# Performance work log

Hardware: AMD Instinct MI355X
Metric: run time of the kernel (lower is better)

Reference implementation:

```python
import jax, jax.numpy as jnp
import numpy as np

NEG_INF = -9.0e15  # matches torch's -9000000000000000.0 mask value
ALPHA = 0.2        # LeakyReLU negative slope


def setup_inputs() -> dict:
    key = jax.random.key(0)
    k1, k2, k3, k4 = jax.random.split(key, 4)
    N, F_in, F_out = 8192, 128, 128
    x = jax.random.normal(k1, (N, F_in), dtype=jnp.float32)
    adj = jax.random.randint(k2, (N, N), 0, 2, dtype=jnp.int32)
    W = jax.random.normal(k3, (F_in, F_out), dtype=jnp.float32) * (1.0 / np.sqrt(F_in))
    a = jax.random.normal(k4, (2 * F_out, 1), dtype=jnp.float32) * (1.0 / np.sqrt(2 * F_out))
    return {"x": x, "adj": adj, "W": W, "a": a}


def reference(x, adj, W, a):
    # h = W(input): [N, F_out]
    h = x @ W
    F_out = h.shape[1]
    # a([h_i || h_j]) = h_i . a[:F] + h_j . a[F:]  -- identical math to the
    # original NxNx2F concat, without materializing it.
    a_src = a[:F_out, 0]   # coefficients on the row (i) node
    a_dst = a[F_out:, 0]   # coefficients on the column (j) node
    s_src = h @ a_src      # [N]
    s_dst = h @ a_dst      # [N]
    e = jax.nn.leaky_relu(s_src[:, None] + s_dst[None, :], negative_slope=ALPHA)  # [N, N]
    e = jnp.where(adj > 0, e, jnp.float32(NEG_INF))
    attention = jax.nn.softmax(e, axis=1)
    # dropout omitted (identity at eval) for a deterministic baseline
    h_prime = attention @ h  # [N, F_out]
    return h_prime
```

## Files before the change

### kernel.cpp

```cpp
#include <hip/hip_runtime.h>

#define N 8192
#define F 128
#define ALPHA 0.2f
#define NSPLIT 4

typedef __attribute__((ext_vector_type(8))) short short8;
typedef __attribute__((ext_vector_type(4))) float f32x4;
typedef unsigned short u16;

__device__ __forceinline__ u16 f2bf(float f) {
    unsigned int u = __float_as_uint(f);
    u += 0x7fff + ((u >> 16) & 1);
    return (u16)(u >> 16);
}

__global__ __launch_bounds__(256) void gemm_h(const float* __restrict__ x,
                                              const float* __restrict__ W,
                                              const float* __restrict__ aa,
                                              u16* __restrict__ hT,
                                              float* __restrict__ ssrc,
                                              float* __restrict__ sdst) {
    __shared__ float xs[32 * 128];
    __shared__ float Wsh[32 * 128];
    const int t = threadIdx.x;
    const int i0 = blockIdx.x * 32;
    const int c4 = (t & 31) * 4;
    const int r8 = t >> 5;

#pragma unroll
    for (int p = 0; p < 4; ++p) {
        int rr = p * 8 + r8;
        *(float4*)&xs[rr * 128 + c4] = *(const float4*)&x[(size_t)(i0 + rr) * 128 + c4];
    }

    const int tx = t & 31, ty = t >> 5;
    const int r0 = ty * 4, c0 = tx * 4;
    float acc[4][4] = {};

    for (int kc = 0; kc < 4; ++kc) {
        __syncthreads();
#pragma unroll
        for (int p = 0; p < 4; ++p) {
            int k = p * 8 + r8;
            *(float4*)&Wsh[k * 128 + c4] = *(const float4*)&W[(kc * 32 + k) * 128 + c4];
        }
        __syncthreads();
#pragma unroll 4
        for (int k = 0; k < 32; k += 4) {
            float xr[4][4];
#pragma unroll
            for (int rr = 0; rr < 4; ++rr)
                *(float4*)xr[rr] = *(const float4*)&xs[(r0 + rr) * 128 + kc * 32 + k];
#pragma unroll
            for (int kk = 0; kk < 4; ++kk) {
                float4 wv = *(const float4*)&Wsh[(k + kk) * 128 + c0];
#pragma unroll
                for (int rr = 0; rr < 4; ++rr) {
                    acc[rr][0] += xr[rr][kk] * wv.x;
                    acc[rr][1] += xr[rr][kk] * wv.y;
                    acc[rr][2] += xr[rr][kk] * wv.z;
                    acc[rr][3] += xr[rr][kk] * wv.w;
                }
            }
        }
    }

#pragma unroll
    for (int rr = 0; rr < 4; ++rr)
#pragma unroll
        for (int cc = 0; cc < 4; ++cc)
            hT[(size_t)(c0 + cc) * N + (i0 + r0 + rr)] = f2bf(acc[rr][cc]);

    float4 asv = *(const float4*)&aa[c0];
    float4 adv = *(const float4*)&aa[F + c0];
#pragma unroll
    for (int rr = 0; rr < 4; ++rr) {
        float vs = acc[rr][0] * asv.x + acc[rr][1] * asv.y + acc[rr][2] * asv.z + acc[rr][3] * asv.w;
        float vd = acc[rr][0] * adv.x + acc[rr][1] * adv.y + acc[rr][2] * adv.z + acc[rr][3] * adv.w;
#pragma unroll
        for (int off = 16; off >= 1; off >>= 1) {
            vs += __shfl_down(vs, off, 32);
            vd += __shfl_down(vd, off, 32);
        }
        if (tx == 0) {
            ssrc[i0 + r0 + rr] = vs;
            sdst[i0 + r0 + rr] = vd;
        }
    }
}

__global__ __launch_bounds__(256, 3) void attn_mfma(const int* __restrict__ adj,
                                                    const u16* __restrict__ hT,
                                                    const float* __restrict__ ssrc,
                                                    const float* __restrict__ sdst,
                                                    float* __restrict__ out,
                                                    float* __restrict__ pacc,
                                                    float* __restrict__ pS) {
    __shared__ short8 wsh[2][4][64];
    __shared__ float srow[2][2][16];

    const int t = threadIdx.x;
    const int w = t >> 6, L = t & 63;
    const int quad = L >> 4, l16 = L & 15;
    const int i0 = blockIdx.x * 32;
    const int split = blockIdx.y;
    const int JW = N / NSPLIT;
    const int jbase = split * JW;
    const int NC = JW / 64;

    const int rt = w & 1, ks = w >> 1;
    const int fragid = rt * 2 + ks;
    const int prow = i0 + rt * 16 + l16;
    const float s_i = ssrc[prow];

    const int* pA = adj + (size_t)prow * N + jbase + ks * 32 + quad * 8;
    const float* pD = sdst + jbase + ks * 32 + quad * 8;
    const u16* pB = hT + (size_t)(w * 32 + l16) * N + jbase + quad * 8;

    f32x4 acc[2][2];
#pragma unroll
    for (int a = 0; a < 2; ++a)
#pragma unroll
        for (int b = 0; b < 2; ++b) acc[a][b] = 0.f;
    float rsum = 0.f;

    auto compute_write = [&](int buf, int4 a0, int4 a1, float4 d0, float4 d1) {
        const int m[8] = {a0.x, a0.y, a0.z, a0.w, a1.x, a1.y, a1.z, a1.w};
        const float d[8] = {d0.x, d0.y, d0.z, d0.w, d1.x, d1.y, d1.z, d1.w};
        float wv[8];
#pragma unroll
        for (int k = 0; k < 8; ++k) {
            float z = s_i + d[k];
            float e = __expf(fmaxf(z, ALPHA * z));
            wv[k] = (m[k] > 0) ? e : 0.f;
        }
        union { unsigned int u[4]; short8 s8; } pk;
        float s = 0.f;
#pragma unroll
        for (int p = 0; p < 4; ++p) {
            unsigned int r;
            asm("v_cvt_pk_bf16_f32 %0, %1, %2" : "=v"(r) : "v"(wv[2 * p]), "v"(wv[2 * p + 1]));
            pk.u[p] = r;
            s += __uint_as_float(r << 16);
            s += __uint_as_float(r & 0xffff0000u);
        }
        rsum += s;
        wsh[buf][fragid][L] = pk.s8;
    };

    int4 aN0 = *(const int4*)(pA);
    int4 aN1 = *(const int4*)(pA + 4);
    int4 aP0 = *(const int4*)(pA + 64);
    int4 aP1 = *(const int4*)(pA + 68);
    float4 dN0 = *(const float4*)(pD);
    float4 dN1 = *(const float4*)(pD + 4);
    compute_write(0, aN0, aN1, dN0, dN1);
    aN0 = aP0; aN1 = aP1;
    aP0 = *(const int4*)(pA + 128);
    aP1 = *(const int4*)(pA + 132);
    dN0 = *(const float4*)(pD + 64);
    dN1 = *(const float4*)(pD + 68);

    short8 Bbuf[2][2];
#pragma unroll
    for (int c2 = 0; c2 < 2; ++c2)
#pragma unroll
        for (int kb = 0; kb < 2; ++kb)
            Bbuf[c2][kb] = *(const short8*)(pB + (size_t)c2 * 16 * N + kb * 32);

    for (int c = 1; c < NC; ++c) {
        __syncthreads();
        const int coff = c * 64;

        short8 Bload[2][2];
#pragma unroll
        for (int c2 = 0; c2 < 2; ++c2)
#pragma unroll
            for (int kb = 0; kb < 2; ++kb)
                Bload[c2][kb] = *(const short8*)(pB + (size_t)c2 * 16 * N + kb * 32 + coff);

        compute_write(c & 1, aN0, aN1, dN0, dN1);

        aN0 = aP0; aN1 = aP1;
        const int ca = (c + 2 < NC) ? c + 2 : NC - 1;
        aP0 = *(const int4*)(pA + ca * 64);
        aP1 = *(const int4*)(pA + ca * 64 + 4);
        const int cd = (c + 1 < NC) ? c + 1 : NC - 1;
        dN0 = *(const float4*)(pD + cd * 64);
        dN1 = *(const float4*)(pD + cd * 64 + 4);

        short8 af[4];
#pragma unroll
        for (int fs = 0; fs < 4; ++fs) af[fs] = wsh[(c - 1) & 1][fs][L];
#pragma unroll
        for (int c2 = 0; c2 < 2; ++c2)
#pragma unroll
            for (int rc = 0; rc < 2; ++rc)
#pragma unroll
                for (int kb = 0; kb < 2; ++kb)
                    acc[c2][rc] = __builtin_amdgcn_mfma_f32_16x16x32_bf16(
                        af[rc * 2 + kb], Bbuf[c2][kb], acc[c2][rc], 0, 0, 0);

#pragma unroll
        for (int c2 = 0; c2 < 2; ++c2)
#pragma unroll
            for (int kb = 0; kb < 2; ++kb) Bbuf[c2][kb] = Bload[c2][kb];
    }

    __syncthreads();
    {
        short8 af[4];
#pragma unroll
        for (int fs = 0; fs < 4; ++fs) af[fs] = wsh[(NC - 1) & 1][fs][L];
#pragma unroll
        for (int c2 = 0; c2 < 2; ++c2)
#pragma unroll
            for (int rc = 0; rc < 2; ++rc)
#pragma unroll
                for (int kb = 0; kb < 2; ++kb)
                    acc[c2][rc] = __builtin_amdgcn_mfma_f32_16x16x32_bf16(
                        af[rc * 2 + kb], Bbuf[c2][kb], acc[c2][rc], 0, 0, 0);
    }

    float* dst = split ? pacc + (size_t)(split - 1) * N * F : out;
#pragma unroll
    for (int c2 = 0; c2 < 2; ++c2) {
        const int col = (w * 2 + c2) * 16 + l16;
#pragma unroll
        for (int rc = 0; rc < 2; ++rc) {
            const int row0 = i0 + rc * 16 + quad * 4;
#pragma unroll
            for (int r = 0; r < 4; ++r)
                dst[(size_t)(row0 + r) * F + col] = acc[c2][rc][r];
        }
    }

    rsum += __shfl_xor(rsum, 16);
    rsum += __shfl_xor(rsum, 32);
    if (L < 16) srow[rt][ks][l16] = rsum;
    __syncthreads();
    if (t < 32) pS[split * N + i0 + t] = srow[t >> 4][0][t & 15] + srow[t >> 4][1][t & 15];
}

__global__ __launch_bounds__(256) void finalize(float* __restrict__ out,
                                                const float* __restrict__ pacc,
                                                const float* __restrict__ pS) {
    const int idx = (blockIdx.x * 256 + threadIdx.x) * 4;
    const int i = idx >> 7;
    const float inv = 1.0f / (pS[i] + pS[N + i] + pS[2 * N + i] + pS[3 * N + i]);
    float4 a0 = *(const float4*)&out[idx];
    float4 a1 = *(const float4*)&pacc[idx];
    float4 a2 = *(const float4*)&pacc[(size_t)N * F + idx];
    float4 a3 = *(const float4*)&pacc[2 * (size_t)N * F + idx];
    float4 o = {(a0.x + a1.x + a2.x + a3.x) * inv,
                (a0.y + a1.y + a2.y + a3.y) * inv,
                (a0.z + a1.z + a2.z + a3.z) * inv,
                (a0.w + a1.w + a2.w + a3.w) * inv};
    *(float4*)&out[idx] = o;
}

extern "C" void kernel_launch(void* const* d_in, const int* in_sizes, int n_in,
                              void* d_out, int out_size, void* d_ws, size_t ws_size,
                              hipStream_t stream) {
    (void)in_sizes; (void)n_in; (void)out_size; (void)ws_size;
    const float* x   = (const float*)d_in[0];
    const int*   adj = (const int*)d_in[1];
    const float* W   = (const float*)d_in[2];
    const float* a   = (const float*)d_in[3];
    float* out = (float*)d_out;

    u16* hT     = (u16*)d_ws;
    float* ssrc = (float*)(hT + (size_t)N * F);
    float* sdst = ssrc + N;
    float* pS   = sdst + N;
    float* pacc = pS + NSPLIT * N;

    gemm_h<<<N / 32, 256, 0, stream>>>(x, W, a, hT, ssrc, sdst);
    attn_mfma<<<dim3(N / 32, NSPLIT), 256, 0, stream>>>(adj, hT, ssrc, sdst, out, pacc, pS);
    finalize<<<(N * F / 4) / 256, 256, 0, stream>>>(out, pacc, pS);
}
```

Baseline: 417.5 us.

## Fuse split-K attention and finalize into one kernel with per-wave K slices

The attention kernel now gives each block 16 rows. Each of its four waves handles a quarter of the columns and keeps all 128 output features in registers, so the shared-memory weight exchange and the per-chunk barriers go away. The partial sums are reduced across waves through shared memory, normalized, and written directly. This removes the global partial-accumulator buffers and the separate finalize kernel. In exchange each wave loads all of hT per chunk with no reuse across waves, uses more registers (occupancy hint dropped to 2), and the grid has more blocks with half the rows each, so B-operand traffic from hT doubles.

```diff
diff --git a/kernel.cpp b/kernel.cpp
--- a/kernel.cpp
+++ b/kernel.cpp
@@ -3,7 +3,6 @@
 #define N 8192
 #define F 128
 #define ALPHA 0.2f
-#define NSPLIT 4
 
 typedef __attribute__((ext_vector_type(8))) short short8;
 typedef __attribute__((ext_vector_type(4))) float f32x4;
@@ -90,42 +89,34 @@
     }
 }
 
-__global__ __launch_bounds__(256, 3) void attn_mfma(const int* __restrict__ adj,
-                                                    const u16* __restrict__ hT,
-                                                    const float* __restrict__ ssrc,
-                                                    const float* __restrict__ sdst,
-                                                    float* __restrict__ out,
-                                                    float* __restrict__ pacc,
-                                                    float* __restrict__ pS) {
-    __shared__ short8 wsh[2][4][64];
-    __shared__ float srow[2][2][16];
+__global__ __launch_bounds__(256, 2) void attn_fused(const int* __restrict__ adj,
+                                                     const u16* __restrict__ hT,
+                                                     const float* __restrict__ ssrc,
+                                                     const float* __restrict__ sdst,
+                                                     float* __restrict__ out) {
+    __shared__ float accsh[4][16][132];
+    __shared__ float srow[4][16];
 
     const int t = threadIdx.x;
     const int w = t >> 6, L = t & 63;
     const int quad = L >> 4, l16 = L & 15;
-    const int i0 = blockIdx.x * 32;
-    const int split = blockIdx.y;
-    const int JW = N / NSPLIT;
-    const int jbase = split * JW;
-    const int NC = JW / 64;
-
-    const int rt = w & 1, ks = w >> 1;
-    const int fragid = rt * 2 + ks;
-    const int prow = i0 + rt * 16 + l16;
+    const int tile0 = blockIdx.x * 16;
+    const int prow = tile0 + l16;
+    const int JW = N / 4;
+    const int jbase = w * JW;
+    const int NC = JW / 32;
+
     const float s_i = ssrc[prow];
-
-    const int* pA = adj + (size_t)prow * N + jbase + ks * 32 + quad * 8;
-    const float* pD = sdst + jbase + ks * 32 + quad * 8;
-    const u16* pB = hT + (size_t)(w * 32 + l16) * N + jbase + quad * 8;
-
-    f32x4 acc[2][2];
-#pragma unroll
-    for (int a = 0; a < 2; ++a)
-#pragma unroll
-        for (int b = 0; b < 2; ++b) acc[a][b] = 0.f;
+    const int* pA = adj + (size_t)prow * N + jbase + quad * 8;
+    const float* pD = sdst + jbase + quad * 8;
+    const u16* pB = hT + (size_t)l16 * N + jbase + quad * 8;
+
+    f32x4 acc[8];
+#pragma unroll
+    for (int cg = 0; cg < 8; ++cg) acc[cg] = 0.f;
     float rsum = 0.f;
 
-    auto compute_write = [&](int buf, int4 a0, int4 a1, float4 d0, float4 d1) {
+    auto mk_frag = [&](int4 a0, int4 a1, float4 d0, float4 d1) -> short8 {
         const int m[8] = {a0.x, a0.y, a0.z, a0.w, a1.x, a1.y, a1.z, a1.w};
         const float d[8] = {d0.x, d0.y, d0.z, d0.w, d1.x, d1.y, d1.z, d1.w};
         float wv[8];
@@ -146,118 +137,73 @@
             s += __uint_as_float(r & 0xffff0000u);
         }
         rsum += s;
-        wsh[buf][fragid][L] = pk.s8;
+        return pk.s8;
     };
 
-    int4 aN0 = *(const int4*)(pA);
-    int4 aN1 = *(const int4*)(pA + 4);
-    int4 aP0 = *(const int4*)(pA + 64);
-    int4 aP1 = *(const int4*)(pA + 68);
-    float4 dN0 = *(const float4*)(pD);
-    float4 dN1 = *(const float4*)(pD + 4);
-    compute_write(0, aN0, aN1, dN0, dN1);
-    aN0 = aP0; aN1 = aP1;
-    aP0 = *(const int4*)(pA + 128);
-    aP1 = *(const int4*)(pA + 132);
-    dN0 = *(const float4*)(pD + 64);
-    dN1 = *(const float4*)(pD + 68);
-
-    short8 Bbuf[2][2];
-#pragma unroll
-    for (int c2 = 0; c2 < 2; ++c2)
-#pragma unroll
-        for (int kb = 0; kb < 2; ++kb)
-            Bbuf[c2][kb] = *(const short8*)(pB + (size_t)c2 * 16 * N + kb * 32);
-
-    for (int c = 1; c < NC; ++c) {
-        __syncthreads();
-        const int coff = c * 64;
-
-        short8 Bload[2][2];
-#pragma unroll
-        for (int c2 = 0; c2 < 2; ++c2)
-#pragma unroll
-            for (int kb = 0; kb < 2; ++kb)
-                Bload[c2][kb] = *(const short8*)(pB + (size_t)c2 * 16 * N + kb * 32 + coff);
-
-        compute_write(c & 1, aN0, aN1, dN0, dN1);
-
-        aN0 = aP0; aN1 = aP1;
-        const int ca = (c + 2 < NC) ? c + 2 : NC - 1;
-        aP0 = *(const int4*)(pA + ca * 64);
-        aP1 = *(const int4*)(pA + ca * 64 + 4);
+    int4 aA0 = *(const int4*)(pA);
+    int4 aA1 = *(const int4*)(pA + 4);
+    int4 aB0 = *(const int4*)(pA + 32);
+    int4 aB1 = *(const int4*)(pA + 36);
+    int4 aC0 = *(const int4*)(pA + 64);
+    int4 aC1 = *(const int4*)(pA + 68);
+    float4 dA0 = *(const float4*)(pD);
+    float4 dA1 = *(const float4*)(pD + 4);
+
+    for (int c = 0; c < NC; ++c) {
+        const int coff = c * 32;
+
+        const int ca = (c + 3 < NC) ? c + 3 : NC - 1;
         const int cd = (c + 1 < NC) ? c + 1 : NC - 1;
-        dN0 = *(const float4*)(pD + cd * 64);
-        dN1 = *(const float4*)(pD + cd * 64 + 4);
-
-        short8 af[4];
-#pragma unroll
-        for (int fs = 0; fs < 4; ++fs) af[fs] = wsh[(c - 1) & 1][fs][L];
-#pragma unroll
-        for (int c2 = 0; c2 < 2; ++c2)
-#pragma unroll
-            for (int rc = 0; rc < 2; ++rc)
-#pragma unroll
-                for (int kb = 0; kb < 2; ++kb)
-                    acc[c2][rc] = __builtin_amdgcn_mfma_f32_16x16x32_bf16(
-                        af[rc * 2 + kb], Bbuf[c2][kb], acc[c2][rc], 0, 0, 0);
-
-#pragma unroll
-        for (int c2 = 0; c2 < 2; ++c2)
-#pragma unroll
-            for (int kb = 0; kb < 2; ++kb) Bbuf[c2][kb] = Bload[c2][kb];
-    }
-
-    __syncthreads();
-    {
-        short8 af[4];
-#pragma unroll
-        for (int fs = 0; fs < 4; ++fs) af[fs] = wsh[(NC - 1) & 1][fs][L];
-#pragma unroll
-        for (int c2 = 0; c2 < 2; ++c2)
-#pragma unroll
-            for (int rc = 0; rc < 2; ++rc)
-#pragma unroll
-                for (int kb = 0; kb < 2; ++kb)
-                    acc[c2][rc] = __builtin_amdgcn_mfma_f32_16x16x32_bf16(
-                        af[rc * 2 + kb], Bbuf[c2][kb], acc[c2][rc], 0, 0, 0);
-    }
-
-    float* dst = split ? pacc + (size_t)(split - 1) * N * F : out;
-#pragma unroll
-    for (int c2 = 0; c2 < 2; ++c2) {
-        const int col = (w * 2 + c2) * 16 + l16;
-#pragma unroll
-        for (int rc = 0; rc < 2; ++rc) {
-            const int row0 = i0 + rc * 16 + quad * 4;
-#pragma unroll
-            for (int r = 0; r < 4; ++r)
-                dst[(size_t)(row0 + r) * F + col] = acc[c2][rc][r];
-        }
+        int4 nA0 = *(const int4*)(pA + ca * 32);
+        int4 nA1 = *(const int4*)(pA + ca * 32 + 4);
+        float4 nD0 = *(const float4*)(pD + cd * 32);
+        float4 nD1 = *(const float4*)(pD + cd * 32 + 4);
+
+        short8 Bv[8];
+#pragma unroll
+        for (int cg = 0; cg < 8; ++cg)
+            Bv[cg] = *(const short8*)(pB + (size_t)cg * 16 * N + coff);
+
+        short8 af = mk_frag(aA0, aA1, dA0, dA1);
+
+#pragma unroll
+        for (int cg = 0; cg < 8; ++cg)
+            acc[cg] = __builtin_amdgcn_mfma_f32_16x16x32_bf16(af, Bv[cg], acc[cg], 0, 0, 0);
+
+        aA0 = aB0; aA1 = aB1;
+        aB0 = aC0; aB1 = aC1;
+        aC0 = nA0; aC1 = nA1;
+        dA0 = nD0; dA1 = nD1;
     }
 
     rsum += __shfl_xor(rsum, 16);
     rsum += __shfl_xor(rsum, 32);
-    if (L < 16) srow[rt][ks][l16] = rsum;
+    if (L < 16) srow[w][l16] = rsum;
+
+#pragma unroll
+    for (int cg = 0; cg < 8; ++cg)
+#pragma unroll
+        for (int r = 0; r < 4; ++r)
+            accsh[w][quad * 4 + r][cg * 16 + l16] = acc[cg][r];
+
     __syncthreads();
-    if (t < 32) pS[split * N + i0 + t] = srow[t >> 4][0][t & 15] + srow[t >> 4][1][t & 15];
-}
-
-__global__ __launch_bounds__(256) void finalize(float* __restrict__ out,
-                                                const float* __restrict__ pacc,
-                                                const float* __restrict__ pS) {
-    const int idx = (blockIdx.x * 256 + threadIdx.x) * 4;
-    const int i = idx >> 7;
-    const float inv = 1.0f / (pS[i] + pS[N + i] + pS[2 * N + i] + pS[3 * N + i]);
-    float4 a0 = *(const float4*)&out[idx];
-    float4 a1 = *(const float4*)&pacc[idx];
-    float4 a2 = *(const float4*)&pacc[(size_t)N * F + idx];
-    float4 a3 = *(const float4*)&pacc[2 * (size_t)N * F + idx];
-    float4 o = {(a0.x + a1.x + a2.x + a3.x) * inv,
-                (a0.y + a1.y + a2.y + a3.y) * inv,
-                (a0.z + a1.z + a2.z + a3.z) * inv,
-                (a0.w + a1.w + a2.w + a3.w) * inv};
-    *(float4*)&out[idx] = o;
+
+#pragma unroll
+    for (int p = 0; p < 2; ++p) {
+        const int fid = t * 2 + p;
+        const int row = fid >> 5;
+        const int c4 = (fid & 31) * 4;
+        float4 s0 = *(const float4*)&accsh[0][row][c4];
+        float4 s1 = *(const float4*)&accsh[1][row][c4];
+        float4 s2 = *(const float4*)&accsh[2][row][c4];
+        float4 s3 = *(const float4*)&accsh[3][row][c4];
+        const float inv = 1.0f / (srow[0][row] + srow[1][row] + srow[2][row] + srow[3][row]);
+        float4 o = {(s0.x + s1.x + s2.x + s3.x) * inv,
+                    (s0.y + s1.y + s2.y + s3.y) * inv,
+                    (s0.z + s1.z + s2.z + s3.z) * inv,
+                    (s0.w + s1.w + s2.w + s3.w) * inv};
+        *(float4*)&out[(size_t)(tile0 + row) * F + c4] = o;
+    }
 }
 
 extern "C" void kernel_launch(void* const* d_in, const int* in_sizes, int n_in,
@@ -273,10 +219,7 @@
     u16* hT     = (u16*)d_ws;
     float* ssrc = (float*)(hT + (size_t)N * F);
     float* sdst = ssrc + N;
-    float* pS   = sdst + N;
-    float* pacc = pS + NSPLIT * N;
 
     gemm_h<<<N / 32, 256, 0, stream>>>(x, W, a, hT, ssrc, sdst);
-    attn_mfma<<<dim3(N / 32, NSPLIT), 256, 0, stream>>>(adj, hT, ssrc, sdst, out, pacc, pS);
-    finalize<<<(N * F / 4) / 256, 256, 0, stream>>>(out, pacc, pS);
-}
+    attn_fused<<<N / 16, 256, 0, stream>>>(adj, hT, ssrc, sdst, out);
+}
```

Result: slower. 485.0 us (+16.2%).

## Double attention row tile to 64 rows per block, reuse B fragments

Applied to the files above, without the earlier changes.

Each block now handles 64 rows instead of 32, with each wave computing weights for two row tiles and all waves doing MFMAs across four row tiles. This halves the number of loads of hT fragments per output row and reduces the block count. The adj prefetch depth drops from two chunks to one, and the MFMA step is issued before the weight computation for the next chunk. The occupancy hint drops from 3 to 2 because register use rises, and the grid is smaller.

```diff
diff --git a/kernel.cpp b/kernel.cpp
--- a/kernel.cpp
+++ b/kernel.cpp
@@ -90,42 +90,45 @@
     }
 }
 
-__global__ __launch_bounds__(256, 3) void attn_mfma(const int* __restrict__ adj,
+__global__ __launch_bounds__(256, 2) void attn_mfma(const int* __restrict__ adj,
                                                     const u16* __restrict__ hT,
                                                     const float* __restrict__ ssrc,
                                                     const float* __restrict__ sdst,
                                                     float* __restrict__ out,
                                                     float* __restrict__ pacc,
                                                     float* __restrict__ pS) {
-    __shared__ short8 wsh[2][4][64];
-    __shared__ float srow[2][2][16];
+    __shared__ short8 wsh[2][8][64];
+    __shared__ float srow[4][2][16];
 
     const int t = threadIdx.x;
     const int w = t >> 6, L = t & 63;
     const int quad = L >> 4, l16 = L & 15;
-    const int i0 = blockIdx.x * 32;
+    const int i0 = blockIdx.x * 64;
     const int split = blockIdx.y;
     const int JW = N / NSPLIT;
     const int jbase = split * JW;
     const int NC = JW / 64;
 
-    const int rt = w & 1, ks = w >> 1;
-    const int fragid = rt * 2 + ks;
-    const int prow = i0 + rt * 16 + l16;
-    const float s_i = ssrc[prow];
-
-    const int* pA = adj + (size_t)prow * N + jbase + ks * 32 + quad * 8;
+    const int ks = w & 1, rp = w >> 1;
+    const int prow0 = i0 + (rp * 2 + 0) * 16 + l16;
+    const int prow1 = i0 + (rp * 2 + 1) * 16 + l16;
+    const float s0 = ssrc[prow0];
+    const float s1 = ssrc[prow1];
+
+    const int* pA0 = adj + (size_t)prow0 * N + jbase + ks * 32 + quad * 8;
+    const int* pA1 = adj + (size_t)prow1 * N + jbase + ks * 32 + quad * 8;
     const float* pD = sdst + jbase + ks * 32 + quad * 8;
     const u16* pB = hT + (size_t)(w * 32 + l16) * N + jbase + quad * 8;
 
-    f32x4 acc[2][2];
+    f32x4 acc[2][4];
 #pragma unroll
     for (int a = 0; a < 2; ++a)
 #pragma unroll
-        for (int b = 0; b < 2; ++b) acc[a][b] = 0.f;
-    float rsum = 0.f;
-
-    auto compute_write = [&](int buf, int4 a0, int4 a1, float4 d0, float4 d1) {
+        for (int b = 0; b < 4; ++b) acc[a][b] = 0.f;
+    float rs0 = 0.f, rs1 = 0.f;
+
+    auto cw = [&](int buf, int fragid, float s_i, float& rsum,
+                  int4 a0, int4 a1, float4 d0, float4 d1) {
         const int m[8] = {a0.x, a0.y, a0.z, a0.w, a1.x, a1.y, a1.z, a1.w};
         const float d[8] = {d0.x, d0.y, d0.z, d0.w, d1.x, d1.y, d1.z, d1.w};
         float wv[8];
@@ -149,25 +152,25 @@
         wsh[buf][fragid][L] = pk.s8;
     };
 
-    int4 aN0 = *(const int4*)(pA);
-    int4 aN1 = *(const int4*)(pA + 4);
-    int4 aP0 = *(const int4*)(pA + 64);
-    int4 aP1 = *(const int4*)(pA + 68);
-    float4 dN0 = *(const float4*)(pD);
-    float4 dN1 = *(const float4*)(pD + 4);
-    compute_write(0, aN0, aN1, dN0, dN1);
-    aN0 = aP0; aN1 = aP1;
-    aP0 = *(const int4*)(pA + 128);
-    aP1 = *(const int4*)(pA + 132);
-    dN0 = *(const float4*)(pD + 64);
-    dN1 = *(const float4*)(pD + 68);
+    const int f0 = (rp * 2 + 0) * 2 + ks;
+    const int f1 = (rp * 2 + 1) * 2 + ks;
+
+    int4 aN00 = *(const int4*)(pA0);     int4 aN01 = *(const int4*)(pA0 + 4);
+    int4 aN10 = *(const int4*)(pA1);     int4 aN11 = *(const int4*)(pA1 + 4);
+    float4 dN0 = *(const float4*)(pD);   float4 dN1 = *(const float4*)(pD + 4);
+    cw(0, f0, s0, rs0, aN00, aN01, dN0, dN1);
+    cw(0, f1, s1, rs1, aN10, aN11, dN0, dN1);
 
     short8 Bbuf[2][2];
 #pragma unroll
     for (int c2 = 0; c2 < 2; ++c2)
 #pragma unroll
         for (int kb = 0; kb < 2; ++kb)
-            Bbuf[c2][kb] = *(const short8*)(pB + (size_t)c2 * 16 * N + kb * 32);
+            Bbuf[c2][kb] = *(const short8*)(pB + (size_t)(c2 * 16) * N + kb * 32);
+
+    aN00 = *(const int4*)(pA0 + 64);  aN01 = *(const int4*)(pA0 + 68);
+    aN10 = *(const int4*)(pA1 + 64);  aN11 = *(const int4*)(pA1 + 68);
+    dN0 = *(const float4*)(pD + 64);  dN1 = *(const float4*)(pD + 68);
 
     for (int c = 1; c < NC; ++c) {
         __syncthreads();
@@ -178,30 +181,31 @@
         for (int c2 = 0; c2 < 2; ++c2)
 #pragma unroll
             for (int kb = 0; kb < 2; ++kb)
-                Bload[c2][kb] = *(const short8*)(pB + (size_t)c2 * 16 * N + kb * 32 + coff);
-
-        compute_write(c & 1, aN0, aN1, dN0, dN1);
-
-        aN0 = aP0; aN1 = aP1;
-        const int ca = (c + 2 < NC) ? c + 2 : NC - 1;
-        aP0 = *(const int4*)(pA + ca * 64);
-        aP1 = *(const int4*)(pA + ca * 64 + 4);
-        const int cd = (c + 1 < NC) ? c + 1 : NC - 1;
-        dN0 = *(const float4*)(pD + cd * 64);
-        dN1 = *(const float4*)(pD + cd * 64 + 4);
-
-        short8 af[4];
-#pragma unroll
-        for (int fs = 0; fs < 4; ++fs) af[fs] = wsh[(c - 1) & 1][fs][L];
-#pragma unroll
-        for (int c2 = 0; c2 < 2; ++c2)
-#pragma unroll
-            for (int rc = 0; rc < 2; ++rc)
+                Bload[c2][kb] = *(const short8*)(pB + (size_t)(c2 * 16) * N + kb * 32 + coff);
+
+        const int cn = (c + 1 < NC) ? c + 1 : NC - 1;
+        int4 aP00 = *(const int4*)(pA0 + cn * 64);  int4 aP01 = *(const int4*)(pA0 + cn * 64 + 4);
+        int4 aP10 = *(const int4*)(pA1 + cn * 64);  int4 aP11 = *(const int4*)(pA1 + cn * 64 + 4);
+        float4 dP0 = *(const float4*)(pD + cn * 64);
+        float4 dP1 = *(const float4*)(pD + cn * 64 + 4);
+
+        short8 af[8];
+#pragma unroll
+        for (int fs = 0; fs < 8; ++fs) af[fs] = wsh[(c - 1) & 1][fs][L];
+#pragma unroll
+        for (int c2 = 0; c2 < 2; ++c2)
+#pragma unroll
+            for (int rt = 0; rt < 4; ++rt)
 #pragma unroll
                 for (int kb = 0; kb < 2; ++kb)
-                    acc[c2][rc] = __builtin_amdgcn_mfma_f32_16x16x32_bf16(
-                        af[rc * 2 + kb], Bbuf[c2][kb], acc[c2][rc], 0, 0, 0);
-
+                    acc[c2][rt] = __builtin_amdgcn_mfma_f32_16x16x32_bf16(
+                        af[rt * 2 + kb], Bbuf[c2][kb], acc[c2][rt], 0, 0, 0);
+
+        cw(c & 1, f0, s0, rs0, aN00, aN01, dN0, dN1);
+        cw(c & 1, f1, s1, rs1, aN10, aN11, dN0, dN1);
+
+        aN00 = aP00; aN01 = aP01; aN10 = aP10; aN11 = aP11;
+        dN0 = dP0; dN1 = dP1;
 #pragma unroll
         for (int c2 = 0; c2 < 2; ++c2)
 #pragma unroll
@@ -210,37 +214,42 @@
 
     __syncthreads();
     {
-        short8 af[4];
-#pragma unroll
-        for (int fs = 0; fs < 4; ++fs) af[fs] = wsh[(NC - 1) & 1][fs][L];
-#pragma unroll
-        for (int c2 = 0; c2 < 2; ++c2)
-#pragma unroll
-            for (int rc = 0; rc < 2; ++rc)
+        short8 af[8];
+#pragma unroll
+        for (int fs = 0; fs < 8; ++fs) af[fs] = wsh[(NC - 1) & 1][fs][L];
+#pragma unroll
+        for (int c2 = 0; c2 < 2; ++c2)
+#pragma unroll
+            for (int rt = 0; rt < 4; ++rt)
 #pragma unroll
                 for (int kb = 0; kb < 2; ++kb)
-                    acc[c2][rc] = __builtin_amdgcn_mfma_f32_16x16x32_bf16(
-                        af[rc * 2 + kb], Bbuf[c2][kb], acc[c2][rc], 0, 0, 0);
+                    acc[c2][rt] = __builtin_amdgcn_mfma_f32_16x16x32_bf16(
+                        af[rt * 2 + kb], Bbuf[c2][kb], acc[c2][rt], 0, 0, 0);
     }
 
     float* dst = split ? pacc + (size_t)(split - 1) * N * F : out;
 #pragma unroll
     for (int c2 = 0; c2 < 2; ++c2) {
-        const int col = (w * 2 + c2) * 16 + l16;
-#pragma unroll
-        for (int rc = 0; rc < 2; ++rc) {
-            const int row0 = i0 + rc * 16 + quad * 4;
+        const int col = w * 32 + c2 * 16 + l16;
+#pragma unroll
+        for (int rt = 0; rt < 4; ++rt) {
+            const int row0 = i0 + rt * 16 + quad * 4;
 #pragma unroll
             for (int r = 0; r < 4; ++r)
-                dst[(size_t)(row0 + r) * F + col] = acc[c2][rc][r];
-        }
-    }
-
-    rsum += __shfl_xor(rsum, 16);
-    rsum += __shfl_xor(rsum, 32);
-    if (L < 16) srow[rt][ks][l16] = rsum;
+                dst[(size_t)(row0 + r) * F + col] = acc[c2][rt][r];
+        }
+    }
+
+    rs0 += __shfl_xor(rs0, 16);
+    rs0 += __shfl_xor(rs0, 32);
+    rs1 += __shfl_xor(rs1, 16);
+    rs1 += __shfl_xor(rs1, 32);
+    if (L < 16) {
+        srow[rp * 2 + 0][ks][l16] = rs0;
+        srow[rp * 2 + 1][ks][l16] = rs1;
+    }
     __syncthreads();
-    if (t < 32) pS[split * N + i0 + t] = srow[t >> 4][0][t & 15] + srow[t >> 4][1][t & 15];
+    if (t < 64) pS[split * N + i0 + t] = srow[t >> 4][0][t & 15] + srow[t >> 4][1][t & 15];
 }
 
 __global__ __launch_bounds__(256) void finalize(float* __restrict__ out,
@@ -277,6 +286,6 @@
     float* pacc = pS + NSPLIT * N;
 
     gemm_h<<<N / 32, 256, 0, stream>>>(x, W, a, hT, ssrc, sdst);
-    attn_mfma<<<dim3(N / 32, NSPLIT), 256, 0, stream>>>(adj, hT, ssrc, sdst, out, pacc, pS);
+    attn_mfma<<<dim3(N / 64, NSPLIT), 256, 0, stream>>>(adj, hT, ssrc, sdst, out, pacc, pS);
     finalize<<<(N * F / 4) / 256, 256, 0, stream>>>(out, pacc, pS);
 }
```

Result: no change. 423.9 us (+1.5%).
